# Kernel optimization log

Measured on AMD Instinct MI355X. Metric: run time of the kernel, lower is better.

Reference implementation:

```python
import jax, jax.numpy as jnp
import numpy as np

DIM = 96
WS = 16            # window_size
OVERLAP = 0.5
UPSCALE = 2
NH = 1             # num_heads
OWIN = int(WS * OVERLAP) + WS          # 24, overlap_win_size
WSU = UPSCALE * WS                     # 32, window_size_up
TABLE = (WSU + OWIN - 1) ** 2          # 3025
PAD = (OWIN - WS) // 2                 # 4


def compute_rpi():
    # Faithful to calculate_rpi_owxra (incl. torch negative-index wraparound -> modulo).
    wsu, cur = WSU, WS + int(OVERLAP * WS)
    a = np.arange(wsu)
    coords_up = np.stack(np.meshgrid(a, a, indexing='ij')).reshape(2, -1)      # (2, wsu^2)
    b = np.arange(cur)
    coords_cur = np.stack(np.meshgrid(b, b, indexing='ij')).reshape(2, -1)     # (2, cur^2)
    rel = coords_cur[:, None, :] - coords_up[:, :, None]                       # (2, wsu^2, cur^2)
    rel = rel.transpose(1, 2, 0).astype(np.int64)
    rel += wsu - cur + 1
    rel[:, :, 0] *= wsu + cur - 1
    idx = rel.sum(-1) % TABLE                                                  # (wsu^2, cur^2)
    return jnp.asarray(idx)


def setup_inputs() -> dict:
    key = jax.random.key(0)
    ks = jax.random.split(key, 6)
    x = jax.random.normal(ks[0], (2, 128, 128, DIM), dtype=jnp.float32)
    x2 = jax.random.normal(ks[1], (128, WSU * WSU, DIM), dtype=jnp.float32)  # (b*nw, 1024, 96)
    Wkv = jax.random.normal(ks[2], (DIM, 2 * DIM), dtype=jnp.float32) * 0.02
    bkv = jnp.zeros((2 * DIM,), dtype=jnp.float32)
    bias_table = jax.random.normal(ks[3], (TABLE, NH), dtype=jnp.float32) * 0.02
    Wproj = jax.random.normal(ks[4], (DIM, DIM), dtype=jnp.float32) * 0.02
    bproj = jnp.zeros((DIM,), dtype=jnp.float32)
    return {"x": x, "x2": x2, "Wkv": Wkv, "bkv": bkv,
            "bias_table": bias_table, "Wproj": Wproj, "bproj": bproj}


def _forward(x, x2, Wkv, bkv, bias_table, Wproj, bproj, rpi):
    b, h, w, c = x.shape
    d = c // NH
    scale = d ** (-0.5)
    kv = x @ Wkv + bkv                                        # (b,h,w,2c); cols [:c]=k, [c:]=v
    p = jnp.pad(kv, ((0, 0), (PAD, PAD), (PAD, PAD), (0, 0)))
    nwh, nww = h // WS, w // WS
    idx_h = (jnp.arange(nwh) * WS)[:, None] + jnp.arange(OWIN)  # (nwh, OWIN)
    idx_w = (jnp.arange(nww) * WS)[:, None] + jnp.arange(OWIN)
    rows = p[:, idx_h]                                        # (b,nwh,OWIN,W',2c)
    wins = rows[:, :, :, idx_w]                               # (b,nwh,OWIN,nww,OWIN,2c)
    wins = wins.transpose(0, 1, 3, 2, 4, 5).reshape(b * nwh * nww, OWIN * OWIN, 2 * c)
    k = wins[..., :c]
    v = wins[..., c:]
    nwb, Q, _ = x2.shape
    K = OWIN * OWIN
    q = x2.reshape(nwb, Q, NH, d).transpose(0, 2, 1, 3) * scale   # (nwb,nh,Q,d)
    kh = k.reshape(nwb, K, NH, d).transpose(0, 2, 1, 3)
    vh = v.reshape(nwb, K, NH, d).transpose(0, 2, 1, 3)
    attn = jnp.einsum('bhqd,bhkd->bhqk', q, kh)
    bias = bias_table[rpi].transpose(2, 0, 1)                  # (nh,Q,K)
    attn = jax.nn.softmax(attn + bias[None], axis=-1)
    out = jnp.einsum('bhqk,bhkd->bhqd', attn, vh)
    out = out.transpose(0, 2, 1, 3).reshape(nwb, Q, c)
    return out @ Wproj + bproj


def reference(x, x2, Wkv, bkv, bias_table, Wproj, bproj):
    rpi = compute_rpi()
    return _forward(x, x2, Wkv, bkv, bias_table, Wproj, bproj, rpi)
```

## Files before the change

kernel.cpp:

```cpp
#include <hip/hip_runtime.h>
#include <hip/hip_bf16.h>
#include <stdint.h>

#define QLEN 1024
#define KLEN 576
#define TABLE_SZ 3025

typedef __attribute__((ext_vector_type(8))) short short8;
typedef __attribute__((ext_vector_type(4))) float floatx4;
typedef __attribute__((ext_vector_type(16))) float floatx16;
typedef __attribute__((ext_vector_type(4))) unsigned short ushort4v;
typedef __attribute__((ext_vector_type(2))) int int2v;

static __device__ __forceinline__ unsigned short f2b(float f) {
    union { float f; unsigned int u; } v; v.f = f;
    return (unsigned short)((v.u + 0x7FFFu + ((v.u >> 16) & 1u)) >> 16);
}
static __device__ __forceinline__ int pk2(float lo, float hi) {
    union { __hip_bfloat162 h; int i; } u;
    u.h = __float22bfloat162_rn(float2{lo, hi});
    return u.i;
}
union W8 { unsigned int u[4]; short8 s8; };

static __device__ __forceinline__ short8 bfrag(int w0, int w1, int w2, int w3) {
    int2v pa = __builtin_amdgcn_permlane32_swap(w0, w2, false, false);
    int2v pb = __builtin_amdgcn_permlane32_swap(w1, w3, false, false);
    W8 w;
    w.u[0] = (unsigned)pa[0];
    w.u[1] = (unsigned)pb[0];
    w.u[2] = (unsigned)pa[1];
    w.u[3] = (unsigned)pb[1];
    return w.s8;
}

__global__ void prep_kernel(const float* __restrict__ Wkv, const float* __restrict__ Wproj,
                            const float* __restrict__ table,
                            unsigned short* __restrict__ WkvT, unsigned short* __restrict__ WprojT,
                            float* __restrict__ biasM) {
    const float LOG2E = 1.4426950408889634f;
    int t0 = blockIdx.x * blockDim.x + threadIdx.x;
    int stride = gridDim.x * blockDim.x;
    for (int i = t0; i < QLEN * KLEN; i += stride) {
        int qi = i / KLEN, kk = i - qi * KLEN;
        int rel0 = kk / 24 - qi / 32 + 9;
        int rel1 = kk % 24 - qi % 32 + 9;
        int s = rel0 * 55 + rel1;
        if (s < 0) s += TABLE_SZ;
        biasM[i] = table[s] * LOG2E;
    }
    for (int i = t0; i < 192 * 96; i += stride) {
        int n = i / 96, k = i - n * 96;
        WkvT[i] = f2b(Wkv[k * 192 + n]);
    }
    for (int i = t0; i < 96 * 96; i += stride) {
        int j = i / 96, d = i - j * 96;
        WprojT[i] = f2b(Wproj[d * 96 + j]);
    }
}

__global__ __launch_bounds__(256) void kv_kernel(const float* __restrict__ x,
        const unsigned short* __restrict__ WkvT, const float* __restrict__ bkv,
        unsigned short* __restrict__ Kpad, unsigned short* __restrict__ Vpad) {
    __shared__ unsigned short xt[64 * 104];
    __shared__ unsigned short vt2[96 * 72];
    int tid = threadIdx.x;
    int mbase = blockIdx.x * 64;
    int bb = mbase >> 14, rem = mbase & 16383;
    int hy = rem >> 7, hx0 = rem & 127;
    #pragma unroll
    for (int it = 0; it < 6; ++it) {
        int c = tid + it * 256;
        int row = c / 24, col4 = (c - row * 24) * 4;
        floatx4 v = *(const floatx4*)(x + (mbase + row) * 96 + col4);
        ushort4v o;
        o[0] = f2b(v[0]); o[1] = f2b(v[1]); o[2] = f2b(v[2]); o[3] = f2b(v[3]);
        *(ushort4v*)&xt[row * 104 + col4] = o;
    }
    __syncthreads();
    int lane = tid & 63, wv = tid >> 6;
    int g = lane >> 4, c16 = lane & 15;
    short8 a[3];
    #pragma unroll
    for (int c = 0; c < 3; ++c)
        a[c] = *(const short8*)&xt[(wv * 16 + c16) * 104 + c * 32 + g * 8];
    floatx4 acc[12];
    #pragma unroll
    for (int nt = 0; nt < 12; ++nt) acc[nt] = (floatx4){0.f, 0.f, 0.f, 0.f};
    #pragma unroll
    for (int nt = 0; nt < 12; ++nt)
        #pragma unroll
        for (int c = 0; c < 3; ++c) {
            short8 b = *(const short8*)(WkvT + (nt * 16 + c16) * 96 + c * 32 + g * 8);
            acc[nt] = __builtin_amdgcn_mfma_f32_16x16x32_bf16(a[c], b, acc[nt], 0, 0, 0);
        }
    #pragma unroll
    for (int nt = 0; nt < 6; ++nt) {
        int col = nt * 16 + c16;
        float bk = bkv[col];
        #pragma unroll
        for (int r = 0; r < 4; ++r) {
            int rowl = wv * 16 + g * 4 + r;
            Kpad[((bb * 136 + hy + 4) * 136 + hx0 + rowl + 4) * 96 + col] = f2b(acc[nt][r] + bk);
        }
    }
    #pragma unroll
    for (int nt = 6; nt < 12; ++nt) {
        int d = nt * 16 + c16 - 96;
        float bk = bkv[96 + d];
        #pragma unroll
        for (int r = 0; r < 4; ++r) {
            int rowl = wv * 16 + g * 4 + r;
            vt2[d * 72 + rowl] = f2b(acc[nt][r] + bk);
        }
    }
    __syncthreads();
    #pragma unroll
    for (int it = 0; it < 3; ++it) {
        int v = tid + it * 256;
        int d = v >> 3, ch = v & 7;
        short8 val = *(const short8*)&vt2[d * 72 + ch * 8];
        *(short8*)(Vpad + ((bb * 96 + d) * 136 + hy + 4) * 136 + hx0 + 4 + ch * 8) = val;
    }
}

__global__ __launch_bounds__(512, 2) void attn_kernel(const float* __restrict__ x2,
        const unsigned short* __restrict__ Kpad, const unsigned short* __restrict__ Vpad,
        const float* __restrict__ biasM,
        const unsigned short* __restrict__ WprojT, const float* __restrict__ bproj,
        float* __restrict__ out) {
    __shared__ unsigned short Kt[2][64 * 104];
    __shared__ unsigned short Vt[2][96 * 72];

    int bid_hw = blockIdx.x;
    int bid = (bid_hw & 7) * 64 + (bid_hw >> 3);
    int wb = bid >> 2, qb = bid & 3;
    int bb = wb >> 6, wy = (wb >> 3) & 7, wx = wb & 7;
    int tid = threadIdx.x, lane = tid & 63, wv = tid >> 6;
    int l31 = lane & 31, h = lane >> 5;
    int qlo = qb * 256 + wv * 32;

    const float qscale = 0.10206207261596577f * 1.4426950408889634f;
    short8 qf[6];
    #pragma unroll
    for (int c = 0; c < 6; ++c) {
        const float* src = x2 + (wb * 1024 + qlo + l31) * 96 + c * 16 + h * 8;
        floatx4 v0 = *(const floatx4*)src;
        floatx4 v1 = *(const floatx4*)(src + 4);
        short8 q;
        #pragma unroll
        for (int i = 0; i < 4; ++i) {
            q[i]     = (short)f2b(v0[i] * qscale);
            q[4 + i] = (short)f2b(v1[i] * qscale);
        }
        qf[c] = q;
    }

    short8 pre[3];
    auto loadpre = [&](int kt) {
        #pragma unroll
        for (int it = 0; it < 3; ++it) {
            int c = tid + it * 512;
            if (c < 768) {
                int kr = c / 12, part = c - kr * 12;
                int kk = kt * 64 + kr;
                int oh = kk / 24, ow = kk - oh * 24;
                pre[it] = *(const short8*)(Kpad + ((bb * 136 + wy * 16 + oh) * 136 + wx * 16 + ow) * 96 + part * 8);
            } else {
                int v = c - 768;
                int d = v >> 3, ch = v & 7;
                int kk0 = kt * 64 + ch * 8;
                int oh = kk0 / 24, ow0 = kk0 - oh * 24;
                pre[it] = *(const short8*)(Vpad + ((bb * 96 + d) * 136 + wy * 16 + oh) * 136 + wx * 16 + ow0);
            }
        }
    };
    auto store_buf = [&](int b) {
        #pragma unroll
        for (int it = 0; it < 3; ++it) {
            int c = tid + it * 512;
            if (c < 768) {
                int kr = c / 12, part = c - kr * 12;
                *(short8*)&Kt[b][kr * 104 + part * 8] = pre[it];
            } else {
                int v = c - 768;
                int d = v >> 3, ch = v & 7;
                *(short8*)&Vt[b][d * 72 + ch * 8] = pre[it];
            }
        }
    };

    floatx16 Oa[3];
    #pragma unroll
    for (int dt = 0; dt < 3; ++dt)
        Oa[dt] = (floatx16){0.f,0.f,0.f,0.f,0.f,0.f,0.f,0.f,0.f,0.f,0.f,0.f,0.f,0.f,0.f,0.f};
    float lp = 0.f;

    loadpre(0);
    store_buf(0);
    loadpre(1);
    __syncthreads();

    for (int kt = 0; kt < 9; ++kt) {
        int cur = kt & 1;
        if (kt < 8) {
            store_buf(cur ^ 1);
            if (kt < 7) loadpre(kt + 2);
        }

        floatx16 s0 = (floatx16){0.f,0.f,0.f,0.f,0.f,0.f,0.f,0.f,0.f,0.f,0.f,0.f,0.f,0.f,0.f,0.f};
        floatx16 s1 = s0;
        __builtin_amdgcn_s_setprio(1);
        #pragma unroll
        for (int c = 0; c < 6; ++c) {
            short8 kf0 = *(const short8*)&Kt[cur][l31 * 104 + c * 16 + h * 8];
            short8 kf1 = *(const short8*)&Kt[cur][(32 + l31) * 104 + c * 16 + h * 8];
            s0 = __builtin_amdgcn_mfma_f32_32x32x16_bf16(kf0, qf[c], s0, 0, 0, 0);
            s1 = __builtin_amdgcn_mfma_f32_32x32x16_bf16(kf1, qf[c], s1, 0, 0, 0);
        }
        __builtin_amdgcn_s_setprio(0);

        const float* brow = biasM + (qlo + l31) * 576 + kt * 64 + h * 4;
        int w[16];
        #pragma unroll
        for (int t = 0; t < 4; ++t) {
            floatx4 bv = *(const floatx4*)(brow + t * 8);
            float p0 = __builtin_amdgcn_exp2f(s0[4 * t + 0] + bv[0]);
            float p1 = __builtin_amdgcn_exp2f(s0[4 * t + 1] + bv[1]);
            float p2 = __builtin_amdgcn_exp2f(s0[4 * t + 2] + bv[2]);
            float p3 = __builtin_amdgcn_exp2f(s0[4 * t + 3] + bv[3]);
            lp += (p0 + p1) + (p2 + p3);
            w[t * 2 + 0] = pk2(p0, p1);
            w[t * 2 + 1] = pk2(p2, p3);
        }
        #pragma unroll
        for (int t = 0; t < 4; ++t) {
            floatx4 bv = *(const floatx4*)(brow + 32 + t * 8);
            float p0 = __builtin_amdgcn_exp2f(s1[4 * t + 0] + bv[0]);
            float p1 = __builtin_amdgcn_exp2f(s1[4 * t + 1] + bv[1]);
            float p2 = __builtin_amdgcn_exp2f(s1[4 * t + 2] + bv[2]);
            float p3 = __builtin_amdgcn_exp2f(s1[4 * t + 3] + bv[3]);
            lp += (p0 + p1) + (p2 + p3);
            w[8 + t * 2 + 0] = pk2(p0, p1);
            w[8 + t * 2 + 1] = pk2(p2, p3);
        }

        #pragma unroll
        for (int kc = 0; kc < 4; ++kc) {
            short8 pf = bfrag(w[kc * 4 + 0], w[kc * 4 + 1], w[kc * 4 + 2], w[kc * 4 + 3]);
            __builtin_amdgcn_s_setprio(1);
            #pragma unroll
            for (int dt = 0; dt < 3; ++dt) {
                short8 vf = *(const short8*)&Vt[cur][(dt * 32 + l31) * 72 + kc * 16 + h * 8];
                Oa[dt] = __builtin_amdgcn_mfma_f32_32x32x16_bf16(vf, pf, Oa[dt], 0, 0, 0);
            }
            __builtin_amdgcn_s_setprio(0);
        }

        __syncthreads();
    }

    lp += __shfl_xor(lp, 32);
    float inv = 1.0f / lp;
    short8 of[6];
    #pragma unroll
    for (int dt = 0; dt < 3; ++dt) {
        int ow[8];
        #pragma unroll
        for (int t = 0; t < 4; ++t) {
            ow[t * 2 + 0] = pk2(Oa[dt][4 * t + 0] * inv, Oa[dt][4 * t + 1] * inv);
            ow[t * 2 + 1] = pk2(Oa[dt][4 * t + 2] * inv, Oa[dt][4 * t + 3] * inv);
        }
        of[dt * 2 + 0] = bfrag(ow[0], ow[1], ow[2], ow[3]);
        of[dt * 2 + 1] = bfrag(ow[4], ow[5], ow[6], ow[7]);
    }
    #pragma unroll
    for (int jt = 0; jt < 3; ++jt) {
        floatx16 acc = (floatx16){0.f,0.f,0.f,0.f,0.f,0.f,0.f,0.f,0.f,0.f,0.f,0.f,0.f,0.f,0.f,0.f};
        #pragma unroll
        for (int st = 0; st < 6; ++st) {
            short8 wf = *(const short8*)(WprojT + (jt * 32 + l31) * 96 + st * 16 + h * 8);
            acc = __builtin_amdgcn_mfma_f32_32x32x16_bf16(wf, of[st], acc, 0, 0, 0);
        }
        int row = wb * 1024 + qlo + l31;
        #pragma unroll
        for (int t = 0; t < 4; ++t) {
            floatx4 bp = *(const floatx4*)(bproj + jt * 32 + t * 8 + h * 4);
            #pragma unroll
            for (int r = 0; r < 4; ++r)
                out[row * 96 + jt * 32 + t * 8 + h * 4 + r] = acc[4 * t + r] + bp[r];
        }
    }
}

extern "C" void kernel_launch(void* const* d_in, const int* in_sizes, int n_in,
                              void* d_out, int out_size, void* d_ws, size_t ws_size,
                              hipStream_t stream) {
    const float* x     = (const float*)d_in[0];
    const float* x2    = (const float*)d_in[1];
    const float* Wkv   = (const float*)d_in[2];
    const float* bkv   = (const float*)d_in[3];
    const float* table = (const float*)d_in[4];
    const float* Wproj = (const float*)d_in[5];
    const float* bproj = (const float*)d_in[6];
    float* out = (float*)d_out;

    char* ws = (char*)d_ws;
    unsigned short* Kpad   = (unsigned short*)ws;
    unsigned short* Vpad   = (unsigned short*)(ws + 7102464);
    float*          biasM  = (float*)(ws + 14204928);
    unsigned short* WkvT   = (unsigned short*)(ws + 16564224);
    unsigned short* WprojT = (unsigned short*)(ws + 16601088);

    hipMemsetAsync(ws, 0, 14204928, stream);
    hipLaunchKernelGGL(prep_kernel, dim3(512), dim3(256), 0, stream,
                       Wkv, Wproj, table, WkvT, WprojT, biasM);
    hipLaunchKernelGGL(kv_kernel, dim3(512), dim3(256), 0, stream,
                       x, WkvT, bkv, Kpad, Vpad);
    hipLaunchKernelGGL(attn_kernel, dim3(512), dim3(512), 0, stream,
                       x2, Kpad, Vpad, biasM, WprojT, bproj, out);
}
```

Baseline: 111.7 us.

## Shrink attention blocks to 256 threads with single-buffered LDS and split score tiles

The attention kernel now runs 1024 blocks of 4 waves, each covering 128 queries, in place of 512 blocks of 8 waves. LDS double buffering is replaced by a single buffer with two barriers per tile plus a register prefetch of the next tile. The QK^T scores are computed in two 32-key halves so only one score accumulator is live at a time. The aim is to cut register and LDS pressure so more blocks fit per CU. The cost is that each block loads the same K/V tiles for fewer queries, doubling K/V traffic, and the extra barrier exposes LDS store latency.

```diff
diff --git a/kernel.cpp b/kernel.cpp
--- a/kernel.cpp
+++ b/kernel.cpp
@@ -124,21 +124,21 @@
     }
 }
 
-__global__ __launch_bounds__(512, 2) void attn_kernel(const float* __restrict__ x2,
+__global__ __launch_bounds__(256, 3) void attn_kernel(const float* __restrict__ x2,
         const unsigned short* __restrict__ Kpad, const unsigned short* __restrict__ Vpad,
         const float* __restrict__ biasM,
         const unsigned short* __restrict__ WprojT, const float* __restrict__ bproj,
         float* __restrict__ out) {
-    __shared__ unsigned short Kt[2][64 * 104];
-    __shared__ unsigned short Vt[2][96 * 72];
+    __shared__ unsigned short Kt[64 * 104];
+    __shared__ unsigned short Vt[96 * 72];
 
     int bid_hw = blockIdx.x;
-    int bid = (bid_hw & 7) * 64 + (bid_hw >> 3);
-    int wb = bid >> 2, qb = bid & 3;
+    int bid = (bid_hw & 7) * 128 + (bid_hw >> 3);
+    int wb = bid >> 3, qb = bid & 7;
     int bb = wb >> 6, wy = (wb >> 3) & 7, wx = wb & 7;
     int tid = threadIdx.x, lane = tid & 63, wv = tid >> 6;
     int l31 = lane & 31, h = lane >> 5;
-    int qlo = qb * 256 + wv * 32;
+    int qlo = qb * 128 + wv * 32;
 
     const float qscale = 0.10206207261596577f * 1.4426950408889634f;
     short8 qf[6];
@@ -156,11 +156,11 @@
         qf[c] = q;
     }
 
-    short8 pre[3];
+    short8 pre[6];
     auto loadpre = [&](int kt) {
         #pragma unroll
-        for (int it = 0; it < 3; ++it) {
-            int c = tid + it * 512;
+        for (int it = 0; it < 6; ++it) {
+            int c = tid + it * 256;
             if (c < 768) {
                 int kr = c / 12, part = c - kr * 12;
                 int kk = kt * 64 + kr;
@@ -175,89 +175,66 @@
             }
         }
     };
-    auto store_buf = [&](int b) {
-        #pragma unroll
-        for (int it = 0; it < 3; ++it) {
-            int c = tid + it * 512;
+
+    floatx16 Oa[3];
+    #pragma unroll
+    for (int dt = 0; dt < 3; ++dt)
+        Oa[dt] = (floatx16){0.f,0.f,0.f,0.f,0.f,0.f,0.f,0.f,0.f,0.f,0.f,0.f,0.f,0.f,0.f,0.f};
+    float lp = 0.f;
+
+    loadpre(0);
+    for (int kt = 0; kt < 9; ++kt) {
+        __syncthreads();
+        #pragma unroll
+        for (int it = 0; it < 6; ++it) {
+            int c = tid + it * 256;
             if (c < 768) {
                 int kr = c / 12, part = c - kr * 12;
-                *(short8*)&Kt[b][kr * 104 + part * 8] = pre[it];
+                *(short8*)&Kt[kr * 104 + part * 8] = pre[it];
             } else {
                 int v = c - 768;
                 int d = v >> 3, ch = v & 7;
-                *(short8*)&Vt[b][d * 72 + ch * 8] = pre[it];
-            }
-        }
-    };
-
-    floatx16 Oa[3];
-    #pragma unroll
-    for (int dt = 0; dt < 3; ++dt)
-        Oa[dt] = (floatx16){0.f,0.f,0.f,0.f,0.f,0.f,0.f,0.f,0.f,0.f,0.f,0.f,0.f,0.f,0.f,0.f};
-    float lp = 0.f;
-
-    loadpre(0);
-    store_buf(0);
-    loadpre(1);
-    __syncthreads();
-
-    for (int kt = 0; kt < 9; ++kt) {
-        int cur = kt & 1;
-        if (kt < 8) {
-            store_buf(cur ^ 1);
-            if (kt < 7) loadpre(kt + 2);
-        }
-
-        floatx16 s0 = (floatx16){0.f,0.f,0.f,0.f,0.f,0.f,0.f,0.f,0.f,0.f,0.f,0.f,0.f,0.f,0.f,0.f};
-        floatx16 s1 = s0;
-        __builtin_amdgcn_s_setprio(1);
-        #pragma unroll
-        for (int c = 0; c < 6; ++c) {
-            short8 kf0 = *(const short8*)&Kt[cur][l31 * 104 + c * 16 + h * 8];
-            short8 kf1 = *(const short8*)&Kt[cur][(32 + l31) * 104 + c * 16 + h * 8];
-            s0 = __builtin_amdgcn_mfma_f32_32x32x16_bf16(kf0, qf[c], s0, 0, 0, 0);
-            s1 = __builtin_amdgcn_mfma_f32_32x32x16_bf16(kf1, qf[c], s1, 0, 0, 0);
-        }
-        __builtin_amdgcn_s_setprio(0);
+                *(short8*)&Vt[d * 72 + ch * 8] = pre[it];
+            }
+        }
+        if (kt < 8) loadpre(kt + 1);
+        __syncthreads();
 
         const float* brow = biasM + (qlo + l31) * 576 + kt * 64 + h * 4;
-        int w[16];
-        #pragma unroll
-        for (int t = 0; t < 4; ++t) {
-            floatx4 bv = *(const floatx4*)(brow + t * 8);
-            float p0 = __builtin_amdgcn_exp2f(s0[4 * t + 0] + bv[0]);
-            float p1 = __builtin_amdgcn_exp2f(s0[4 * t + 1] + bv[1]);
-            float p2 = __builtin_amdgcn_exp2f(s0[4 * t + 2] + bv[2]);
-            float p3 = __builtin_amdgcn_exp2f(s0[4 * t + 3] + bv[3]);
-            lp += (p0 + p1) + (p2 + p3);
-            w[t * 2 + 0] = pk2(p0, p1);
-            w[t * 2 + 1] = pk2(p2, p3);
-        }
-        #pragma unroll
-        for (int t = 0; t < 4; ++t) {
-            floatx4 bv = *(const floatx4*)(brow + 32 + t * 8);
-            float p0 = __builtin_amdgcn_exp2f(s1[4 * t + 0] + bv[0]);
-            float p1 = __builtin_amdgcn_exp2f(s1[4 * t + 1] + bv[1]);
-            float p2 = __builtin_amdgcn_exp2f(s1[4 * t + 2] + bv[2]);
-            float p3 = __builtin_amdgcn_exp2f(s1[4 * t + 3] + bv[3]);
-            lp += (p0 + p1) + (p2 + p3);
-            w[8 + t * 2 + 0] = pk2(p0, p1);
-            w[8 + t * 2 + 1] = pk2(p2, p3);
-        }
-
-        #pragma unroll
-        for (int kc = 0; kc < 4; ++kc) {
-            short8 pf = bfrag(w[kc * 4 + 0], w[kc * 4 + 1], w[kc * 4 + 2], w[kc * 4 + 3]);
+        #pragma unroll
+        for (int half = 0; half < 2; ++half) {
+            floatx16 s = (floatx16){0.f,0.f,0.f,0.f,0.f,0.f,0.f,0.f,0.f,0.f,0.f,0.f,0.f,0.f,0.f,0.f};
             __builtin_amdgcn_s_setprio(1);
             #pragma unroll
-            for (int dt = 0; dt < 3; ++dt) {
-                short8 vf = *(const short8*)&Vt[cur][(dt * 32 + l31) * 72 + kc * 16 + h * 8];
-                Oa[dt] = __builtin_amdgcn_mfma_f32_32x32x16_bf16(vf, pf, Oa[dt], 0, 0, 0);
+            for (int c = 0; c < 6; ++c) {
+                short8 kf = *(const short8*)&Kt[(half * 32 + l31) * 104 + c * 16 + h * 8];
+                s = __builtin_amdgcn_mfma_f32_32x32x16_bf16(kf, qf[c], s, 0, 0, 0);
             }
             __builtin_amdgcn_s_setprio(0);
-        }
-
-        __syncthreads();
+            int w[8];
+            #pragma unroll
+            for (int t = 0; t < 4; ++t) {
+                floatx4 bv = *(const floatx4*)(brow + half * 32 + t * 8);
+                float p0 = __builtin_amdgcn_exp2f(s[4 * t + 0] + bv[0]);
+                float p1 = __builtin_amdgcn_exp2f(s[4 * t + 1] + bv[1]);
+                float p2 = __builtin_amdgcn_exp2f(s[4 * t + 2] + bv[2]);
+                float p3 = __builtin_amdgcn_exp2f(s[4 * t + 3] + bv[3]);
+                lp += (p0 + p1) + (p2 + p3);
+                w[t * 2 + 0] = pk2(p0, p1);
+                w[t * 2 + 1] = pk2(p2, p3);
+            }
+            #pragma unroll
+            for (int kc = 0; kc < 2; ++kc) {
+                short8 pf = bfrag(w[kc * 4 + 0], w[kc * 4 + 1], w[kc * 4 + 2], w[kc * 4 + 3]);
+                __builtin_amdgcn_s_setprio(1);
+                #pragma unroll
+                for (int dt = 0; dt < 3; ++dt) {
+                    short8 vf = *(const short8*)&Vt[(dt * 32 + l31) * 72 + (half * 2 + kc) * 16 + h * 8];
+                    Oa[dt] = __builtin_amdgcn_mfma_f32_32x32x16_bf16(vf, pf, Oa[dt], 0, 0, 0);
+                }
+                __builtin_amdgcn_s_setprio(0);
+            }
+        }
     }
 
     lp += __shfl_xor(lp, 32);
@@ -317,6 +294,6 @@
                        Wkv, Wproj, table, WkvT, WprojT, biasM);
     hipLaunchKernelGGL(kv_kernel, dim3(512), dim3(256), 0, stream,
                        x, WkvT, bkv, Kpad, Vpad);
-    hipLaunchKernelGGL(attn_kernel, dim3(512), dim3(512), 0, stream,
+    hipLaunchKernelGGL(attn_kernel, dim3(1024), dim3(256), 0, stream,
                        x2, Kpad, Vpad, biasM, WprojT, bproj, out);
 }
```

Result: no change. 111.0 us (-0.6%).
